# Kernel tuning notes

Measured on AMD Instinct MI355X. Metric: run time of the kernel, lower is better.

## Reference

```python
import jax, jax.numpy as jnp
import numpy as np

K = 20
EPS = 1e-5  # BatchNorm eps
SLOPE = 0.2  # LeakyReLU negative slope


def _lrelu(y):
    return jnp.where(y > 0, y, SLOPE * y)


def _knn_idx(x):
    # x: [B, C, N] -> idx [B, N, K] of nearest neighbors (largest of negative sq dist)
    inner = -2.0 * jnp.einsum('bcn,bcm->bnm', x, x)
    xx = jnp.sum(x * x, axis=1)  # [B, N]
    pd = -xx[:, :, None] - inner - xx[:, None, :]  # [B, N, N]
    return jax.lax.top_k(pd, K)[1]


def _graph_feature(x):
    # x: [B, C, N] -> [B, 2C, N, K] = cat(neighbor - center, center)
    idx = _knn_idx(x)
    xt = jnp.transpose(x, (0, 2, 1))  # [B, N, C]
    nb = jax.vmap(lambda f, i: f[i])(xt, idx)  # [B, N, K, C]
    ctr = xt[:, :, None, :]
    feat = jnp.concatenate([nb - ctr, jnp.broadcast_to(ctr, nb.shape)], axis=-1)
    return jnp.transpose(feat, (0, 3, 1, 2))


def _bn(y, p, ch_axis):
    g, b, m, v = p[0], p[1], p[2], p[3]
    shape = [1] * y.ndim
    shape[ch_axis] = -1
    scale = (g / jnp.sqrt(v + EPS)).reshape(shape)
    return (y - m.reshape(shape)) * scale + b.reshape(shape)


def _conv_block(x, w, bn):
    f = _graph_feature(x)  # [B, 2C_in, N, K]
    y = jnp.einsum('bcnk,oc->bonk', f, w)  # 1x1 conv, no bias
    y = _lrelu(_bn(y, bn, 1))
    return jnp.max(y, axis=-1)  # max over K neighbors -> [B, C_out, N]


def setup_inputs() -> dict:
    key = jax.random.key(0)
    ks = jax.random.split(key, 20)
    B, N = 8, 1024
    inp = {
        'x': jax.random.normal(ks[0], (B, 3, N), jnp.float32),
        'w0': jax.random.normal(ks[1], (64, 6), jnp.float32) * 0.1,
        'w1': jax.random.normal(ks[2], (64, 128), jnp.float32) * 0.1,
        'w2': jax.random.normal(ks[3], (128, 128), jnp.float32) * 0.1,
        'w3': jax.random.normal(ks[4], (256, 256), jnp.float32) * 0.1,
        'bn0': jax.random.uniform(ks[5], (4, 64), jnp.float32) + 0.1,
        'bn1': jax.random.uniform(ks[6], (4, 64), jnp.float32) + 0.1,
        'bn2': jax.random.uniform(ks[7], (4, 128), jnp.float32) + 0.1,
        'bn3': jax.random.uniform(ks[8], (4, 256), jnp.float32) + 0.1,
        'we': jax.random.normal(ks[9], (1024, 512), jnp.float32) * 0.05,
        'bne': jax.random.uniform(ks[10], (4, 1024), jnp.float32) + 0.1,
        'wf0': jax.random.normal(ks[11], (512, 2048), jnp.float32) * 0.02,
        'bnf0': jax.random.uniform(ks[12], (4, 512), jnp.float32) + 0.1,
        'wf1': jax.random.normal(ks[13], (256, 512), jnp.float32) * 0.05,
        'bnf1': jax.random.uniform(ks[14], (4, 256), jnp.float32) + 0.1,
        'wfin': jax.random.normal(ks[15], (64, 256), jnp.float32) * 0.05,
        'bfin': jax.random.normal(ks[16], (64,), jnp.float32) * 0.05,
    }
    return inp


def reference(x, w0, w1, w2, w3, bn0, bn1, bn2, bn3, we, bne, wf0, bnf0, wf1, bnf1, wfin, bfin):
    B = x.shape[0]
    x1 = _conv_block(x, w0, bn0)   # [B, 64, N]
    x2 = _conv_block(x1, w1, bn1)  # [B, 64, N]
    x3 = _conv_block(x2, w2, bn2)  # [B, 128, N]
    x4 = _conv_block(x3, w3, bn3)  # [B, 256, N]
    cat = jnp.concatenate([x1, x2, x3, x4], axis=1)  # [B, 512, N]
    e = _lrelu(_bn(jnp.einsum('bcn,oc->bon', cat, we), bne, 1))  # [B, 1024, N]
    p1 = jnp.max(e, axis=-1)
    p2 = jnp.mean(e, axis=-1)
    h = jnp.concatenate([p1, p2], axis=1)  # [B, 2048]
    h = _lrelu(_bn(h @ wf0.T, bnf0, 1))  # [B, 512]; dropout is eval-mode identity
    h = _lrelu(_bn(h @ wf1.T, bnf1, 1))  # [B, 256]
    return h @ wfin.T + bfin  # [B, 64]
```

## Files before the change

kernel.cpp:

```cpp
#include <hip/hip_runtime.h>
#include <math.h>

#define N_PTS 1024
#define BATCH 8
#define KNN 20
#define EPSB 1e-5f
#define SLOPE 0.2f

typedef __attribute__((ext_vector_type(8))) short short8;
typedef __attribute__((ext_vector_type(4))) float f32x4;
typedef unsigned short ushort_t;
typedef unsigned long long u64;

#define LDS_U32(p) ((__attribute__((address_space(3))) unsigned int*)(p))
#define GLB_U32(p) ((const __attribute__((address_space(1))) unsigned int*)(p))

__device__ __forceinline__ void glds16(const ushort_t* g, ushort_t* l) {
    __builtin_amdgcn_global_load_lds(GLB_U32(g), LDS_U32(l), 16, 0, 0);
}

__device__ __forceinline__ float lrelu(float y) { return y > 0.f ? y : SLOPE * y; }

__device__ __forceinline__ ushort_t f2bf(float f) {
    union { float f; unsigned u; } v; v.f = f;
    unsigned r = v.u + 0x7FFF + ((v.u >> 16) & 1);
    return (ushort_t)(r >> 16);
}
__device__ __forceinline__ float bf2f(ushort_t h) {
    union { unsigned u; float f; } v; v.u = ((unsigned)h) << 16; return v.f;
}

__device__ __forceinline__ void wprep_one(const float* __restrict__ w, float* __restrict__ wpt,
                                          int C, int Cout, int g) {
    int M2 = 2 * Cout;
    if (g >= C * M2) return;
    int c = g / M2, m = g - c * M2;
    float v;
    if (m < Cout) v = w[(size_t)m * 2 * C + c];
    else { int o = m - Cout; v = w[(size_t)o * 2 * C + C + c] - w[(size_t)o * 2 * C + c]; }
    wpt[(size_t)c * M2 + m] = v;
}

__device__ __forceinline__ void wext_one(const float* __restrict__ w, ushort_t* __restrict__ Wext,
                                         int C, int Cout, int g, int lg2C) {
    int M2 = 2 * Cout;
    if (g >= C * M2) return;
    int m = g >> lg2C, c = g & (C - 1);
    float v;
    if (m < Cout) v = w[(size_t)m * 2 * C + c];
    else { int o = m - Cout; v = w[(size_t)o * 2 * C + C + c] - w[(size_t)o * 2 * C + c]; }
    ushort_t h = f2bf(v);
    float r1 = v - bf2f(h);
    ushort_t md = f2bf(r1);
    ushort_t lo = f2bf(r1 - bf2f(md));
    ushort_t* dst = Wext + (size_t)m * 3 * C + c;
    dst[0] = h; dst[C] = md; dst[2 * C] = lo;
}

__global__ void prep_kernel(const float* __restrict__ we, ushort_t* __restrict__ weh,
                            const float* __restrict__ w0, float* __restrict__ wpt0,
                            const float* __restrict__ w1, ushort_t* __restrict__ Wext1,
                            const float* __restrict__ w2, ushort_t* __restrict__ Wext2,
                            const float* __restrict__ w3, ushort_t* __restrict__ Wext3) {
    int bx = blockIdx.x, tid = threadIdx.x;
    if (bx < 512) {
        int g = bx * 256 + tid;
        float4 v = ((const float4*)we)[g];
        ushort4 o;
        o.x = f2bf(v.x); o.y = f2bf(v.y); o.z = f2bf(v.z); o.w = f2bf(v.w);
        ((ushort4*)weh)[g] = o;
    } else if (bx < 514) {
        wprep_one(w0, wpt0, 3, 64, (bx - 512) * 256 + tid);
    } else if (bx < 546) {
        wext_one(w1, Wext1, 64, 64, (bx - 514) * 256 + tid, 6);
    } else if (bx < 610) {
        wext_one(w2, Wext2, 64, 128, (bx - 546) * 256 + tid, 6);
    } else {
        wext_one(w3, Wext3, 128, 256, (bx - 610) * 256 + tid, 7);
    }
}

__global__ void __launch_bounds__(256)
split_kernel(const float* __restrict__ in, ushort_t* __restrict__ xT3,
             float* __restrict__ xxv, int C, int bstride) {
    int b = blockIdx.z, nt = blockIdx.x;
    int tid = threadIdx.x;
    __shared__ float tile[64][65];
    const float* ib = in + (size_t)b * bstride;
    int S3 = 3 * C;
    float xxa = 0.f;
    for (int ct = 0; ct < C; ct += 64) {
        __syncthreads();
        for (int qq = 0; qq < 16; qq++) {
            int e = qq * 256 + tid;
            int c = e >> 6, n = e & 63;
            tile[c][n] = ib[(size_t)(ct + c) * N_PTS + nt * 64 + n];
        }
        __syncthreads();
        if (tid < 64) {
            for (int c = 0; c < 64; c++) { float v = tile[c][tid]; xxa += v * v; }
        }
        for (int qq = 0; qq < 16; qq++) {
            int e = qq * 256 + tid;
            int n = e >> 6, c = e & 63;
            float v = tile[c][n];
            ushort_t h = f2bf(v);
            float r1 = v - bf2f(h);
            ushort_t md = f2bf(r1);
            ushort_t lo = f2bf(r1 - bf2f(md));
            ushort_t* dst = xT3 + ((size_t)b * N_PTS + nt * 64 + n) * S3 + ct + c;
            dst[0] = h; dst[C] = md; dst[2 * C] = lo;
        }
    }
    if (tid < 64) xxv[b * N_PTS + nt * 64 + tid] = xxa;
}

__global__ void __launch_bounds__(256)
pdabv_mfma(const ushort_t* __restrict__ xT3, const ushort_t* __restrict__ Wext,
           const float* __restrict__ xxv,
           float* __restrict__ pd, float* __restrict__ A, float* __restrict__ Bv,
           int C, int lg2C, int Cout) {
    int b = blockIdx.z, mt = blockIdx.y, nt = blockIdx.x;
    int tid = threadIdx.x;
    int wv = tid >> 6, lane = tid & 63, q = lane >> 4, lr = lane & 15;
    int mblk = wv >> 1, nblk = wv & 1;
    int srow = lane >> 2;
    int scol = (lane & 3) * 8;
    const int S3 = 3 * C;
    bool isPd = (mt < 8);
    const ushort_t* Abase = isPd ? (xT3 + ((size_t)b * N_PTS + mt * 128) * S3)
                                 : (Wext + (size_t)(mt - 8) * 128 * S3);
    const ushort_t* Bbase = xT3 + ((size_t)b * N_PTS + nt * 128) * S3;
    __shared__ __align__(16) ushort_t sA[128 * 32];
    __shared__ __align__(16) ushort_t sB[128 * 32];
    __shared__ float sxxA[128], sxxB[128];
    if (isPd && tid < 128) {
        sxxA[tid] = xxv[b * N_PTS + mt * 128 + tid];
        sxxB[tid] = xxv[b * N_PTS + nt * 128 + tid];
    }
    f32x4 acc[4][4] = {};
    const int pA6[6] = {0, 0, 1, 1, 0, 2};
    const int pB6[6] = {0, 1, 0, 1, 2, 0};
    const int pA3[3] = {0, 0, 1};
    const int pB3[3] = {0, 1, 0};
    int nseg = isPd ? 6 : 3;
    for (int ks = 0; ks < nseg * C; ks += 32) {
        int seg = ks >> lg2C;
        int kl = ks & (C - 1);
        int aoff = (isPd ? pA6[seg] : pA3[seg]) * C + kl;
        int boff = (isPd ? pB6[seg] : pB3[seg]) * C + kl;
        __syncthreads();
        #pragma unroll
        for (int h = 0; h < 2; h++) {
            int chunk = wv + h * 4;
            int row = chunk * 16 + srow;
            glds16(Abase + (size_t)row * S3 + aoff + scol, sA + chunk * 512);
            glds16(Bbase + (size_t)row * S3 + boff + scol, sB + chunk * 512);
        }
        __syncthreads();
        short8 af[4], bfr[4];
        for (int mi = 0; mi < 4; mi++)
            af[mi] = *(const short8*)&sA[(mblk * 64 + mi * 16 + lr) * 32 + q * 8];
        for (int ni = 0; ni < 4; ni++)
            bfr[ni] = *(const short8*)&sB[(nblk * 64 + ni * 16 + lr) * 32 + q * 8];
        for (int mi = 0; mi < 4; mi++)
            for (int ni = 0; ni < 4; ni++)
                acc[mi][ni] = __builtin_amdgcn_mfma_f32_16x16x32_bf16(af[mi], bfr[ni], acc[mi][ni], 0, 0, 0);
    }
    if (isPd) {
        for (int mi = 0; mi < 4; mi++)
        for (int r = 0; r < 4; r++) {
            int row = mblk * 64 + mi * 16 + q * 4 + r;
            float xr = sxxA[row];
            float* prow = pd + ((size_t)(b * N_PTS + mt * 128 + row)) * N_PTS + nt * 128;
            for (int ni = 0; ni < 4; ni++) {
                int col = nblk * 64 + ni * 16 + lr;
                prow[col] = 2.f * acc[mi][ni][r] - xr - sxxB[col];
            }
        }
    } else {
        for (int mi = 0; mi < 4; mi++)
        for (int r = 0; r < 4; r++) {
            int rowm = (mt - 8) * 128 + mblk * 64 + mi * 16 + q * 4 + r;
            float* dst = (rowm < Cout) ? (A + ((size_t)b * Cout + rowm) * N_PTS)
                                       : (Bv + ((size_t)b * Cout + rowm - Cout) * N_PTS);
            for (int ni = 0; ni < 4; ni++) {
                int col = nblk * 64 + ni * 16 + lr;
                dst[nt * 128 + col] = acc[mi][ni][r];
            }
        }
    }
}

__global__ void __launch_bounds__(256)
pdabv_valu(const float* __restrict__ x, const float* __restrict__ wpt,
           float* __restrict__ pd, float* __restrict__ A, float* __restrict__ Bv,
           int C, int Cout, int bstride) {
    int b = blockIdx.z;
    int nt = blockIdx.y;
    int bx = blockIdx.x;
    int tid = threadIdx.x;
    int tx = tid & 15, ty = tid >> 4;
    int n0 = nt * 128;
    __shared__ float sU0[16][128];
    __shared__ float sU1[16][128];
    __shared__ float sXX[256];
    const float* xb = x + (size_t)b * bstride;
    float acc[8][8] = {};
    if (bx < 8) {
        int m0 = bx * 128;
        float xxa = 0.f;
        for (int c0 = 0; c0 < C; c0 += 16) {
            for (int q = 0; q < 2; q++) {
                int f = q * 256 + tid;
                int r = f >> 5, col = (f & 31) * 4;
                int c = c0 + r;
                float4 vn = {0.f, 0.f, 0.f, 0.f}, vm = {0.f, 0.f, 0.f, 0.f};
                if (c < C) {
                    vn = *(const float4*)&xb[(size_t)c * N_PTS + n0 + col];
                    vm = *(const float4*)&xb[(size_t)c * N_PTS + m0 + col];
                }
                *(float4*)&sU0[r][col] = vn;
                *(float4*)&sU1[r][col] = vm;
            }
            __syncthreads();
            if (tid < 128) {
                for (int k = 0; k < 16; k++) { float v = sU0[k][tid]; xxa += v * v; }
            } else {
                int u = tid - 128;
                for (int k = 0; k < 16; k++) { float v = sU1[k][u]; xxa += v * v; }
            }
            for (int k = 0; k < 16; k++) {
                float4 a0 = *(const float4*)&sU0[k][ty * 4];
                float4 a1 = *(const float4*)&sU0[k][64 + ty * 4];
                float4 b0 = *(const float4*)&sU1[k][tx * 4];
                float4 b1 = *(const float4*)&sU1[k][64 + tx * 4];
                float av[8] = {a0.x, a0.y, a0.z, a0.w, a1.x, a1.y, a1.z, a1.w};
                float bw[8] = {b0.x, b0.y, b0.z, b0.w, b1.x, b1.y, b1.z, b1.w};
                for (int i = 0; i < 8; i++)
                    for (int j = 0; j < 8; j++) acc[i][j] += av[i] * bw[j];
            }
            __syncthreads();
        }
        sXX[tid] = xxa;
        __syncthreads();
        float xnv[8], xmv[8];
        for (int i = 0; i < 8; i++) xnv[i] = sXX[(i >> 2) * 64 + ty * 4 + (i & 3)];
        for (int j = 0; j < 8; j++) xmv[j] = sXX[128 + (j >> 2) * 64 + tx * 4 + (j & 3)];
        for (int i = 0; i < 8; i++) {
            int n = n0 + (i >> 2) * 64 + ty * 4 + (i & 3);
            float* prow = pd + ((size_t)(b * N_PTS + n)) * N_PTS;
            for (int jh = 0; jh < 2; jh++) {
                float4 o;
                o.x = 2.f * acc[i][jh * 4 + 0] - xnv[i] - xmv[jh * 4 + 0];
                o.y = 2.f * acc[i][jh * 4 + 1] - xnv[i] - xmv[jh * 4 + 1];
                o.z = 2.f * acc[i][jh * 4 + 2] - xnv[i] - xmv[jh * 4 + 2];
                o.w = 2.f * acc[i][jh * 4 + 3] - xnv[i] - xmv[jh * 4 + 3];
                *(float4*)&prow[m0 + jh * 64 + tx * 4] = o;
            }
        }
    } else {
        int m0 = (bx - 8) * 128;
        int M2 = 2 * Cout;
        for (int c0 = 0; c0 < C; c0 += 16) {
            for (int q = 0; q < 2; q++) {
                int f = q * 256 + tid;
                int r = f >> 5, col = (f & 31) * 4;
                int c = c0 + r;
                float4 vw = {0.f, 0.f, 0.f, 0.f}, vx = {0.f, 0.f, 0.f, 0.f};
                if (c < C) {
                    vw = *(const float4*)&wpt[(size_t)c * M2 + m0 + col];
                    vx = *(const float4*)&xb[(size_t)c * N_PTS + n0 + col];
                }
                *(float4*)&sU0[r][col] = vw;
                *(float4*)&sU1[r][col] = vx;
            }
            __syncthreads();
            for (int k = 0; k < 16; k++) {
                float4 a0 = *(const float4*)&sU0[k][ty * 4];
                float4 a1 = *(const float4*)&sU0[k][64 + ty * 4];
                float4 b0 = *(const float4*)&sU1[k][tx * 4];
                float4 b1 = *(const float4*)&sU1[k][64 + tx * 4];
                float av[8] = {a0.x, a0.y, a0.z, a0.w, a1.x, a1.y, a1.z, a1.w};
                float bw[8] = {b0.x, b0.y, b0.z, b0.w, b1.x, b1.y, b1.z, b1.w};
                for (int i = 0; i < 8; i++)
                    for (int j = 0; j < 8; j++) acc[i][j] += av[i] * bw[j];
            }
            __syncthreads();
        }
        for (int i = 0; i < 8; i++) {
            int rowm = m0 + (i >> 2) * 64 + ty * 4 + (i & 3);
            float* dst = (rowm < Cout) ? (A + ((size_t)b * Cout + rowm) * N_PTS)
                                       : (Bv + ((size_t)b * Cout + rowm - Cout) * N_PTS);
            for (int jh = 0; jh < 2; jh++) {
                float4 o;
                o.x = acc[i][jh * 4 + 0];
                o.y = acc[i][jh * 4 + 1];
                o.z = acc[i][jh * 4 + 2];
                o.w = acc[i][jh * 4 + 3];
                *(float4*)&dst[n0 + jh * 64 + tx * 4] = o;
            }
        }
    }
}

__global__ void __launch_bounds__(256)
topk_kernel(const float* __restrict__ pd, int* __restrict__ idx) {
    int wid = threadIdx.x >> 6;
    int row = blockIdx.x * 4 + wid;
    int lane = threadIdx.x & 63;
    __shared__ u64 Sk[4][64];
    const float* p = pd + (size_t)row * N_PTS;
    float v[16];
    for (int q = 0; q < 4; q++) {
        float4 t = *(const float4*)&p[lane * 16 + q * 4];
        v[q * 4 + 0] = t.x; v[q * 4 + 1] = t.y; v[q * 4 + 2] = t.z; v[q * 4 + 3] = t.w;
    }
    float lmax = v[0];
    #pragma unroll
    for (int j = 1; j < 16; j++) lmax = fmaxf(lmax, v[j]);
    float s = lmax;
    #pragma unroll
    for (int k = 2; k <= 64; k <<= 1) {
        #pragma unroll
        for (int j = k >> 1; j > 0; j >>= 1) {
            float o = __shfl_xor(s, j, 64);
            bool takeMin = (((lane & k) == 0) == ((lane & j) == 0));
            float mn = fminf(s, o), mx = fmaxf(s, o);
            s = takeMin ? mn : mx;
        }
    }
    float tp = __shfl(s, 44, 64);
    unsigned hm = 0;
    #pragma unroll
    for (int j = 0; j < 16; j++) hm |= (v[j] >= tp ? 1u : 0u) << j;
    int cnt = __popc(hm);
    int incl = cnt;
    #pragma unroll
    for (int d = 1; d < 64; d <<= 1) {
        int o = __shfl_up(incl, d, 64);
        if (lane >= d) incl += o;
    }
    int total = __shfl(incl, 63, 64);
    int pos = incl - cnt;
    if (total <= 64) {
        #pragma unroll
        for (int j = 0; j < 16; j++) {
            if (hm & (1u << j)) {
                unsigned u = __float_as_uint(v[j]);
                unsigned msk = ((unsigned)((int)u >> 31)) | 0x80000000u;
                Sk[wid][pos] = ((u64)(u ^ msk) << 32) | (unsigned)(1023 - (lane * 16 + j));
                pos++;
            }
        }
        u64 key = (lane < total) ? Sk[wid][lane] : 0ull;
        #pragma unroll
        for (int k = 2; k <= 64; k <<= 1) {
            #pragma unroll
            for (int j = k >> 1; j > 0; j >>= 1) {
                u64 o = __shfl_xor(key, j, 64);
                bool takeMin = (((lane & k) == 0) == ((lane & j) == 0));
                bool sgt = key > o;
                key = (sgt != takeMin) ? key : o;
            }
        }
        if (lane >= 44) {
            int m = 1023 - (int)(unsigned)(key & 0xFFFFFFFFu);
            idx[row * KNN + (63 - lane)] = m;
        }
    } else {
        for (int kk = 0; kk < KNN; kk++) {
            float bv = v[0]; int bj = 0;
            #pragma unroll
            for (int j = 1; j < 16; j++) if (v[j] > bv) { bv = v[j]; bj = j; }
            int bi = lane * 16 + bj;
            for (int d = 32; d > 0; d >>= 1) {
                float ov = __shfl_down(bv, d, 64);
                int oi = __shfl_down(bi, d, 64);
                if (ov > bv || (ov == bv && oi < bi)) { bv = ov; bi = oi; }
            }
            bi = __shfl(bi, 0, 64);
            if ((bi >> 4) == lane) {
                #pragma unroll
                for (int j = 0; j < 16; j++) if (j == (bi & 15)) v[j] = -INFINITY;
            }
            if (lane == 0) idx[row * KNN + kk] = bi;
        }
    }
}

__global__ void __launch_bounds__(256)
gmax_kernel(const float* __restrict__ A, const float* __restrict__ Bv,
            const int* __restrict__ idx, const float* __restrict__ bnp,
            float* __restrict__ out, int Cout, int outStrideB) {
    int b = blockIdx.z;
    int n0 = blockIdx.x * 64;
    int o0 = blockIdx.y * 4;
    int tid = threadIdx.x;
    __shared__ int sidx[64 * 21];
    __shared__ float sA[4][N_PTS];
    for (int t = tid; t < 64 * KNN; t += 256) {
        int nl = t / KNN, k = t - nl * KNN;
        sidx[nl * 21 + k] = idx[(b * N_PTS + n0) * KNN + t];
    }
    const float* Abase = A + ((size_t)b * Cout + o0) * N_PTS;
    for (int q = 0; q < 4; q++) {
        int f = q * 256 + tid;
        int r = f >> 8, c4 = (f & 255) * 4;
        *(float4*)&sA[r][c4] = *(const float4*)&Abase[(size_t)r * N_PTS + c4];
    }
    __syncthreads();
    int nl = tid & 63, ol = tid >> 6;
    float best = -INFINITY;
    #pragma unroll
    for (int k = 0; k < KNN; k++) {
        int j = sidx[nl * 21 + k];
        best = fmaxf(best, sA[ol][j]);
    }
    int o = o0 + ol;
    int n = n0 + nl;
    float pre = best + Bv[((size_t)b * Cout + o) * N_PTS + n];
    float g = bnp[o], bb = bnp[Cout + o], m = bnp[2 * Cout + o], vv = bnp[3 * Cout + o];
    float scale = g / sqrtf(vv + EPSB);
    out[(size_t)b * outStrideB + (size_t)o * N_PTS + n] = lrelu((pre - m) * scale + bb);
}

__global__ void catT_kernel(const float* __restrict__ cat, ushort_t* __restrict__ catT) {
    int b = blockIdx.z, ct = blockIdx.y, nt = blockIdx.x;
    int tid = threadIdx.x;
    __shared__ float tile[64][65];
    const float* cb = cat + (size_t)b * 512 * N_PTS;
    for (int q = 0; q < 16; q++) {
        int e = q * 256 + tid;
        int c = e >> 6, n = e & 63;
        tile[c][n] = cb[(size_t)(ct * 64 + c) * N_PTS + nt * 64 + n];
    }
    __syncthreads();
    for (int q = 0; q < 16; q++) {
        int e = q * 256 + tid;
        int n = e >> 6, c = e & 63;
        catT[((size_t)b * N_PTS + nt * 64 + n) * 512 + ct * 64 + c] = f2bf(tile[c][n]);
    }
}

__global__ void __launch_bounds__(256)
gemm6_mfma(const ushort_t* __restrict__ weh, const ushort_t* __restrict__ catT,
           const float* __restrict__ bne,
           float* __restrict__ pmax, float* __restrict__ psum) {
    int b = blockIdx.z, ot = blockIdx.y, nt = blockIdx.x;
    int tid = threadIdx.x;
    int wv = tid >> 6, lane = tid & 63, q = lane >> 4, lr = lane & 15;
    int mblk = wv >> 1, nblk = wv & 1;
    int srow = lane >> 2, scol = (lane & 3) * 8;
    __shared__ __align__(16) ushort_t sA[128 * 32];
    __shared__ __align__(16) ushort_t sB[128 * 32];
    __shared__ float sa[128], sc[128];
    __shared__ float redmax[128][2], redsum[128][2];
    int o0 = ot * 128, n0 = nt * 128;
    if (tid < 128) {
        int o = o0 + tid;
        float g = bne[o], bb = bne[1024 + o], m = bne[2048 + o], vv = bne[3072 + o];
        float scale = g / sqrtf(vv + EPSB);
        sa[tid] = scale; sc[tid] = bb - m * scale;
    }
    f32x4 acc[4][4] = {};
    const ushort_t* cT = catT + (size_t)b * N_PTS * 512;
    for (int k0 = 0; k0 < 512; k0 += 32) {
        __syncthreads();
        #pragma unroll
        for (int h = 0; h < 2; h++) {
            int chunk = wv + h * 4;
            int row = chunk * 16 + srow;
            glds16(weh + (size_t)(o0 + row) * 512 + k0 + scol, sA + chunk * 512);
            glds16(cT  + (size_t)(n0 + row) * 512 + k0 + scol, sB + chunk * 512);
        }
        __syncthreads();
        short8 af[4], bfr[4];
        for (int mi = 0; mi < 4; mi++)
            af[mi] = *(const short8*)&sA[(mblk * 64 + mi * 16 + lr) * 32 + q * 8];
        for (int ni = 0; ni < 4; ni++)
            bfr[ni] = *(const short8*)&sB[(nblk * 64 + ni * 16 + lr) * 32 + q * 8];
        for (int mi = 0; mi < 4; mi++)
            for (int ni = 0; ni < 4; ni++)
                acc[mi][ni] = __builtin_amdgcn_mfma_f32_16x16x32_bf16(af[mi], bfr[ni], acc[mi][ni], 0, 0, 0);
    }
    for (int mi = 0; mi < 4; mi++) {
        for (int r = 0; r < 4; r++) {
            int row = mblk * 64 + mi * 16 + q * 4 + r;
            float a = sa[row], c = sc[row];
            float mx = -INFINITY, sm = 0.f;
            for (int ni = 0; ni < 4; ni++) {
                float y = lrelu(acc[mi][ni][r] * a + c);
                mx = fmaxf(mx, y); sm += y;
            }
            for (int msk = 1; msk < 16; msk <<= 1) {
                mx = fmaxf(mx, __shfl_xor(mx, msk, 16));
                sm += __shfl_xor(sm, msk, 16);
            }
            if (lr == 0) { redmax[row][nblk] = mx; redsum[row][nblk] = sm; }
        }
    }
    __syncthreads();
    if (tid < 128) {
        float mx = fmaxf(redmax[tid][0], redmax[tid][1]);
        float sm = redsum[tid][0] + redsum[tid][1];
        int o = o0 + tid;
        pmax[((size_t)(b * 1024 + o)) * 8 + nt] = mx;
        psum[((size_t)(b * 1024 + o)) * 8 + nt] = sm;
    }
}

__global__ void pool_reduce_kernel(const float* __restrict__ pmax, const float* __restrict__ psum,
                                   float* __restrict__ h0) {
    int g = blockIdx.x * 256 + threadIdx.x;
    int b = g >> 10, o = g & 1023;
    float mx = -INFINITY, sm = 0.f;
    for (int t = 0; t < 8; t++) { mx = fmaxf(mx, pmax[g * 8 + t]); sm += psum[g * 8 + t]; }
    h0[(size_t)b * 2048 + o] = mx;
    h0[(size_t)b * 2048 + 1024 + o] = sm * (1.0f / 1024.0f);
}

__global__ void fc_kernel(const float* __restrict__ in, const float* __restrict__ w,
                          const float* __restrict__ bnp, const float* __restrict__ bias,
                          float* __restrict__ out, int Cin, int Cout, int mode) {
    int blk = blockIdx.x;
    int b = blk / Cout, o = blk % Cout;
    int lane = threadIdx.x;
    const float* inb = in + (size_t)b * Cin;
    const float* wo = w + (size_t)o * Cin;
    float acc = 0.f;
    for (int c = lane; c < Cin; c += 64) acc += inb[c] * wo[c];
    for (int s = 32; s > 0; s >>= 1) acc += __shfl_down(acc, s, 64);
    if (lane == 0) {
        float y = acc;
        if (mode == 0) {
            float g = bnp[o], bb = bnp[Cout + o], m = bnp[2 * Cout + o], vv = bnp[3 * Cout + o];
            y = lrelu((y - m) * (g / sqrtf(vv + EPSB)) + bb);
        } else {
            y += bias[o];
        }
        out[(size_t)b * Cout + o] = y;
    }
}

extern "C" void kernel_launch(void* const* d_in, const int* in_sizes, int n_in,
                              void* d_out, int out_size, void* d_ws, size_t ws_size,
                              hipStream_t stream) {
    const float* x    = (const float*)d_in[0];
    const float* w0   = (const float*)d_in[1];
    const float* w1   = (const float*)d_in[2];
    const float* w2   = (const float*)d_in[3];
    const float* w3   = (const float*)d_in[4];
    const float* bn0  = (const float*)d_in[5];
    const float* bn1  = (const float*)d_in[6];
    const float* bn2  = (const float*)d_in[7];
    const float* bn3  = (const float*)d_in[8];
    const float* we   = (const float*)d_in[9];
    const float* bne  = (const float*)d_in[10];
    const float* wf0  = (const float*)d_in[11];
    const float* bnf0 = (const float*)d_in[12];
    const float* wf1  = (const float*)d_in[13];
    const float* bnf1 = (const float*)d_in[14];
    const float* wfin = (const float*)d_in[15];
    const float* bfin = (const float*)d_in[16];

    float* ws = (float*)d_ws;
    size_t off = 0;
    float* cat  = ws + off; off += (size_t)BATCH * 512 * N_PTS;
    float* pd   = ws + off; off += (size_t)BATCH * N_PTS * N_PTS;
    float* A    = ws + off; off += (size_t)BATCH * 256 * N_PTS;
    float* Bv   = ws + off; off += (size_t)BATCH * 256 * N_PTS;
    float* pmax = ws + off; off += (size_t)BATCH * N_PTS * 8;
    float* psum = ws + off; off += (size_t)BATCH * N_PTS * 8;
    float* h0   = ws + off; off += (size_t)BATCH * 2048;
    float* h1   = ws + off; off += (size_t)BATCH * 512;
    float* h2   = ws + off; off += (size_t)BATCH * 256;
    float* xxv  = ws + off; off += (size_t)BATCH * N_PTS;
    int*   idx  = (int*)(ws + off); off += (size_t)BATCH * N_PTS * KNN;
    ushort_t* weh  = (ushort_t*)(ws + off); off += (size_t)(1024 * 512) / 2;
    ushort_t* catT = (ushort_t*)(ws + off); off += (size_t)BATCH * N_PTS * 512 / 2;
    ushort_t* xT3  = (ushort_t*)(ws + off); off += (size_t)BATCH * N_PTS * 3 * 128 / 2;
    ushort_t* Wext1 = (ushort_t*)(ws + off); off += (size_t)(128 * 3 * 64) / 2;
    ushort_t* Wext2 = (ushort_t*)(ws + off); off += (size_t)(256 * 3 * 64) / 2;
    ushort_t* Wext3 = (ushort_t*)(ws + off); off += (size_t)(512 * 3 * 128) / 2;
    float* wpt0 = ws + off; off += 3 * 128;

    const int CSTR = 512 * N_PTS;
    const int topkBlocks = BATCH * N_PTS / 4;

    prep_kernel<<<866, 256, 0, stream>>>(we, weh, w0, wpt0, w1, Wext1, w2, Wext2, w3, Wext3);

    pdabv_valu<<<dim3(9, 8, BATCH), 256, 0, stream>>>(x, wpt0, pd, A, Bv, 3, 64, 3 * N_PTS);
    topk_kernel<<<topkBlocks, 256, 0, stream>>>(pd, idx);
    gmax_kernel<<<dim3(16, 16, BATCH), 256, 0, stream>>>(A, Bv, idx, bn0, cat, 64, CSTR);

    split_kernel<<<dim3(16, 1, BATCH), 256, 0, stream>>>(cat, xT3, xxv, 64, CSTR);
    pdabv_mfma<<<dim3(8, 9, BATCH), 256, 0, stream>>>(xT3, Wext1, xxv, pd, A, Bv, 64, 6, 64);
    topk_kernel<<<topkBlocks, 256, 0, stream>>>(pd, idx);
    gmax_kernel<<<dim3(16, 16, BATCH), 256, 0, stream>>>(A, Bv, idx, bn1, cat + 64 * N_PTS, 64, CSTR);

    split_kernel<<<dim3(16, 1, BATCH), 256, 0, stream>>>(cat + 64 * N_PTS, xT3, xxv, 64, CSTR);
    pdabv_mfma<<<dim3(8, 10, BATCH), 256, 0, stream>>>(xT3, Wext2, xxv, pd, A, Bv, 64, 6, 128);
    topk_kernel<<<topkBlocks, 256, 0, stream>>>(pd, idx);
    gmax_kernel<<<dim3(16, 32, BATCH), 256, 0, stream>>>(A, Bv, idx, bn2, cat + 128 * N_PTS, 128, CSTR);

    split_kernel<<<dim3(16, 1, BATCH), 256, 0, stream>>>(cat + 128 * N_PTS, xT3, xxv, 128, CSTR);
    pdabv_mfma<<<dim3(8, 12, BATCH), 256, 0, stream>>>(xT3, Wext3, xxv, pd, A, Bv, 128, 7, 256);
    topk_kernel<<<topkBlocks, 256, 0, stream>>>(pd, idx);
    gmax_kernel<<<dim3(16, 64, BATCH), 256, 0, stream>>>(A, Bv, idx, bn3, cat + 256 * N_PTS, 256, CSTR);

    catT_kernel<<<dim3(16, 8, BATCH), 256, 0, stream>>>(cat, catT);
    gemm6_mfma<<<dim3(8, 8, BATCH), 256, 0, stream>>>(weh, catT, bne, pmax, psum);
    pool_reduce_kernel<<<32, 256, 0, stream>>>(pmax, psum, h0);

    fc_kernel<<<BATCH * 512, 64, 0, stream>>>(h0, wf0, bnf0, nullptr, h1, 2048, 512, 0);
    fc_kernel<<<BATCH * 256, 64, 0, stream>>>(h1, wf1, bnf1, nullptr, h2, 512, 256, 0);
    fc_kernel<<<BATCH * 64, 64, 0, stream>>>(h2, wfin, nullptr, bfin, (float*)d_out, 256, 64, 1);
}
```

Before: 338.8 us.

## Fuse split and catT transposes into gmax epilogue

The gmax kernel now writes its output directly into the transposed bf16 catT buffer and into the three-way bf16 split buffer for the next layer. It also accumulates squared norms into per-layer xx buffers via atomics, so split_kernel and catT_kernel are removed. This drops four launches and the re-reads of cat. The fused writes are scattered 2-byte stores with a large stride, which may coalesce poorly, and a memset is added to zero the atomic accumulators.

```diff
diff --git a/kernel.cpp b/kernel.cpp
--- a/kernel.cpp
+++ b/kernel.cpp
@@ -80,40 +80,6 @@
     }
 }
 
-__global__ void __launch_bounds__(256)
-split_kernel(const float* __restrict__ in, ushort_t* __restrict__ xT3,
-             float* __restrict__ xxv, int C, int bstride) {
-    int b = blockIdx.z, nt = blockIdx.x;
-    int tid = threadIdx.x;
-    __shared__ float tile[64][65];
-    const float* ib = in + (size_t)b * bstride;
-    int S3 = 3 * C;
-    float xxa = 0.f;
-    for (int ct = 0; ct < C; ct += 64) {
-        __syncthreads();
-        for (int qq = 0; qq < 16; qq++) {
-            int e = qq * 256 + tid;
-            int c = e >> 6, n = e & 63;
-            tile[c][n] = ib[(size_t)(ct + c) * N_PTS + nt * 64 + n];
-        }
-        __syncthreads();
-        if (tid < 64) {
-            for (int c = 0; c < 64; c++) { float v = tile[c][tid]; xxa += v * v; }
-        }
-        for (int qq = 0; qq < 16; qq++) {
-            int e = qq * 256 + tid;
-            int n = e >> 6, c = e & 63;
-            float v = tile[c][n];
-            ushort_t h = f2bf(v);
-            float r1 = v - bf2f(h);
-            ushort_t md = f2bf(r1);
-            ushort_t lo = f2bf(r1 - bf2f(md));
-            ushort_t* dst = xT3 + ((size_t)b * N_PTS + nt * 64 + n) * S3 + ct + c;
-            dst[0] = h; dst[C] = md; dst[2 * C] = lo;
-        }
-    }
-    if (tid < 64) xxv[b * N_PTS + nt * 64 + tid] = xxa;
-}
 
 __global__ void __launch_bounds__(256)
 pdabv_mfma(const ushort_t* __restrict__ xT3, const ushort_t* __restrict__ Wext,
@@ -124,8 +90,7 @@
     int tid = threadIdx.x;
     int wv = tid >> 6, lane = tid & 63, q = lane >> 4, lr = lane & 15;
     int mblk = wv >> 1, nblk = wv & 1;
-    int srow = lane >> 2;
-    int scol = (lane & 3) * 8;
+    int srow = lane >> 2, scol = (lane & 3) * 8;
     const int S3 = 3 * C;
     bool isPd = (mt < 8);
     const ushort_t* Abase = isPd ? (xT3 + ((size_t)b * N_PTS + mt * 128) * S3)
@@ -392,13 +357,17 @@
 __global__ void __launch_bounds__(256)
 gmax_kernel(const float* __restrict__ A, const float* __restrict__ Bv,
             const int* __restrict__ idx, const float* __restrict__ bnp,
-            float* __restrict__ out, int Cout, int outStrideB) {
+            float* __restrict__ out, int Cout, int outStrideB,
+            ushort_t* __restrict__ catT, int chbase,
+            ushort_t* __restrict__ xT3next, int Cnext,
+            float* __restrict__ xxnext) {
     int b = blockIdx.z;
     int n0 = blockIdx.x * 64;
     int o0 = blockIdx.y * 4;
     int tid = threadIdx.x;
     __shared__ int sidx[64 * 21];
     __shared__ float sA[4][N_PTS];
+    __shared__ float xred[4][65];
     for (int t = tid; t < 64 * KNN; t += 256) {
         int nl = t / KNN, k = t - nl * KNN;
         sidx[nl * 21 + k] = idx[(b * N_PTS + n0) * KNN + t];
@@ -422,24 +391,24 @@
     float pre = best + Bv[((size_t)b * Cout + o) * N_PTS + n];
     float g = bnp[o], bb = bnp[Cout + o], m = bnp[2 * Cout + o], vv = bnp[3 * Cout + o];
     float scale = g / sqrtf(vv + EPSB);
-    out[(size_t)b * outStrideB + (size_t)o * N_PTS + n] = lrelu((pre - m) * scale + bb);
-}
-
-__global__ void catT_kernel(const float* __restrict__ cat, ushort_t* __restrict__ catT) {
-    int b = blockIdx.z, ct = blockIdx.y, nt = blockIdx.x;
-    int tid = threadIdx.x;
-    __shared__ float tile[64][65];
-    const float* cb = cat + (size_t)b * 512 * N_PTS;
-    for (int q = 0; q < 16; q++) {
-        int e = q * 256 + tid;
-        int c = e >> 6, n = e & 63;
-        tile[c][n] = cb[(size_t)(ct * 64 + c) * N_PTS + nt * 64 + n];
-    }
-    __syncthreads();
-    for (int q = 0; q < 16; q++) {
-        int e = q * 256 + tid;
-        int n = e >> 6, c = e & 63;
-        catT[((size_t)b * N_PTS + nt * 64 + n) * 512 + ct * 64 + c] = f2bf(tile[c][n]);
+    float y = lrelu((pre - m) * scale + bb);
+    out[(size_t)b * outStrideB + (size_t)o * N_PTS + n] = y;
+    catT[((size_t)b * N_PTS + n) * 512 + chbase + o] = f2bf(y);
+    if (xT3next) {
+        ushort_t h = f2bf(y);
+        float r1 = y - bf2f(h);
+        ushort_t md = f2bf(r1);
+        ushort_t lo = f2bf(r1 - bf2f(md));
+        ushort_t* dst = xT3next + ((size_t)b * N_PTS + n) * 3 * Cnext + o;
+        dst[0] = h; dst[Cnext] = md; dst[2 * Cnext] = lo;
+    }
+    if (xxnext) {
+        xred[ol][nl] = y * y;
+        __syncthreads();
+        if (tid < 64) {
+            float s = xred[0][tid] + xred[1][tid] + xred[2][tid] + xred[3][tid];
+            atomicAdd(&xxnext[b * N_PTS + n0 + tid], s);
+        }
     }
 }
 
@@ -575,11 +544,15 @@
     float* h0   = ws + off; off += (size_t)BATCH * 2048;
     float* h1   = ws + off; off += (size_t)BATCH * 512;
     float* h2   = ws + off; off += (size_t)BATCH * 256;
-    float* xxv  = ws + off; off += (size_t)BATCH * N_PTS;
+    float* xx1  = ws + off; off += (size_t)BATCH * N_PTS;
+    float* xx2  = ws + off; off += (size_t)BATCH * N_PTS;
+    float* xx3  = ws + off; off += (size_t)BATCH * N_PTS;
     int*   idx  = (int*)(ws + off); off += (size_t)BATCH * N_PTS * KNN;
     ushort_t* weh  = (ushort_t*)(ws + off); off += (size_t)(1024 * 512) / 2;
     ushort_t* catT = (ushort_t*)(ws + off); off += (size_t)BATCH * N_PTS * 512 / 2;
-    ushort_t* xT3  = (ushort_t*)(ws + off); off += (size_t)BATCH * N_PTS * 3 * 128 / 2;
+    ushort_t* xT3a = (ushort_t*)(ws + off); off += (size_t)BATCH * N_PTS * 3 * 64 / 2;
+    ushort_t* xT3b = (ushort_t*)(ws + off); off += (size_t)BATCH * N_PTS * 3 * 64 / 2;
+    ushort_t* xT3c = (ushort_t*)(ws + off); off += (size_t)BATCH * N_PTS * 3 * 128 / 2;
     ushort_t* Wext1 = (ushort_t*)(ws + off); off += (size_t)(128 * 3 * 64) / 2;
     ushort_t* Wext2 = (ushort_t*)(ws + off); off += (size_t)(256 * 3 * 64) / 2;
     ushort_t* Wext3 = (ushort_t*)(ws + off); off += (size_t)(512 * 3 * 128) / 2;
@@ -588,31 +561,32 @@
     const int CSTR = 512 * N_PTS;
     const int topkBlocks = BATCH * N_PTS / 4;
 
+    hipMemsetAsync(xx1, 0, 3 * (size_t)BATCH * N_PTS * sizeof(float), stream);
+
     prep_kernel<<<866, 256, 0, stream>>>(we, weh, w0, wpt0, w1, Wext1, w2, Wext2, w3, Wext3);
 
     pdabv_valu<<<dim3(9, 8, BATCH), 256, 0, stream>>>(x, wpt0, pd, A, Bv, 3, 64, 3 * N_PTS);
     topk_kernel<<<topkBlocks, 256, 0, stream>>>(pd, idx);
-    gmax_kernel<<<dim3(16, 16, BATCH), 256, 0, stream>>>(A, Bv, idx, bn0, cat, 64, CSTR);
-
-    split_kernel<<<dim3(16, 1, BATCH), 256, 0, stream>>>(cat, xT3, xxv, 64, CSTR);
-    pdabv_mfma<<<dim3(8, 9, BATCH), 256, 0, stream>>>(xT3, Wext1, xxv, pd, A, Bv, 64, 6, 64);
+    gmax_kernel<<<dim3(16, 16, BATCH), 256, 0, stream>>>(A, Bv, idx, bn0, cat, 64, CSTR,
+                                                         catT, 0, xT3a, 64, xx1);
+
+    pdabv_mfma<<<dim3(8, 9, BATCH), 256, 0, stream>>>(xT3a, Wext1, xx1, pd, A, Bv, 64, 6, 64);
     topk_kernel<<<topkBlocks, 256, 0, stream>>>(pd, idx);
-    gmax_kernel<<<dim3(16, 16, BATCH), 256, 0, stream>>>(A, Bv, idx, bn1, cat + 64 * N_PTS, 64, CSTR);
-
-    split_kernel<<<dim3(16, 1, BATCH), 256, 0, stream>>>(cat + 64 * N_PTS, xT3, xxv, 64, CSTR);
-    pdabv_mfma<<<dim3(8, 10, BATCH), 256, 0, stream>>>(xT3, Wext2, xxv, pd, A, Bv, 64, 6, 128);
+    gmax_kernel<<<dim3(16, 16, BATCH), 256, 0, stream>>>(A, Bv, idx, bn1, cat + 64 * N_PTS, 64, CSTR,
+                                                         catT, 64, xT3b, 64, xx2);
+
+    pdabv_mfma<<<dim3(8, 10, BATCH), 256, 0, stream>>>(xT3b, Wext2, xx2, pd, A, Bv, 64, 6, 128);
     topk_kernel<<<topkBlocks, 256, 0, stream>>>(pd, idx);
-    gmax_kernel<<<dim3(16, 32, BATCH), 256, 0, stream>>>(A, Bv, idx, bn2, cat + 128 * N_PTS, 128, CSTR);
-
-    split_kernel<<<dim3(16, 1, BATCH), 256, 0, stream>>>(cat + 128 * N_PTS, xT3, xxv, 128, CSTR);
-    pdabv_mfma<<<dim3(8, 12, BATCH), 256, 0, stream>>>(xT3, Wext3, xxv, pd, A, Bv, 128, 7, 256);
+    gmax_kernel<<<dim3(16, 32, BATCH), 256, 0, stream>>>(A, Bv, idx, bn2, cat + 128 * N_PTS, 128, CSTR,
+                                                         catT, 128, xT3c, 128, xx3);
+
+    pdabv_mfma<<<dim3(8, 12, BATCH), 256, 0, stream>>>(xT3c, Wext3, xx3, pd, A, Bv, 128, 7, 256);
     topk_kernel<<<topkBlocks, 256, 0, stream>>>(pd, idx);
-    gmax_kernel<<<dim3(16, 64, BATCH), 256, 0, stream>>>(A, Bv, idx, bn3, cat + 256 * N_PTS, 256, CSTR);
-
-    catT_kernel<<<dim3(16, 8, BATCH), 256, 0, stream>>>(cat, catT);
+    gmax_kernel<<<dim3(16, 64, BATCH), 256, 0, stream>>>(A, Bv, idx, bn3, cat + 256 * N_PTS, 256, CSTR,
+                                                         catT, 256, (ushort_t*)nullptr, 0, (float*)nullptr);
+
     gemm6_mfma<<<dim3(8, 8, BATCH), 256, 0, stream>>>(weh, catT, bne, pmax, psum);
     pool_reduce_kernel<<<32, 256, 0, stream>>>(pmax, psum, h0);
-
     fc_kernel<<<BATCH * 512, 64, 0, stream>>>(h0, wf0, bnf0, nullptr, h1, 2048, 512, 0);
     fc_kernel<<<BATCH * 256, 64, 0, stream>>>(h1, wf1, bnf1, nullptr, h2, 512, 256, 0);
     fc_kernel<<<BATCH * 64, 64, 0, stream>>>(h2, wfin, nullptr, bfin, (float*)d_out, 256, 64, 1);
```

New measurement: 339.8 us. About the same (+0.3%).
